# Kernel optimization log

Measured on AMD Instinct MI355X. Metric: run time of the kernel, lower is better.

Reference implementation:

```python
import jax, jax.numpy as jnp
import numpy as np

BN_EPS = 1e-5

def conv1x1(w, b, x):
    # w: [O, C], b: [O], x: [B, C, H, W] -> [B, O, H, W]
    return jnp.einsum('oc,bchw->bohw', w, x) + b[None, :, None, None]

def setup_inputs() -> dict:
    key = jax.random.key(0)
    ks = jax.random.split(key, 11)
    C, inter = 256, 128
    B, H, W = 16, 64, 32
    s = 0.05
    return {
        'x': jax.random.normal(ks[0], (B, C, H, W), jnp.float32),
        'g_w': jax.random.normal(ks[1], (inter, C), jnp.float32) * s,
        'g_b': jax.random.normal(ks[2], (inter,), jnp.float32) * s,
        'theta_w': jax.random.normal(ks[3], (inter, C), jnp.float32) * s,
        'theta_b': jax.random.normal(ks[4], (inter,), jnp.float32) * s,
        'phi_w': jax.random.normal(ks[5], (inter, C), jnp.float32) * s,
        'phi_b': jax.random.normal(ks[6], (inter,), jnp.float32) * s,
        'W_w': jax.random.normal(ks[7], (C, inter), jnp.float32) * s,
        'W_b': jax.random.normal(ks[8], (C,), jnp.float32) * s,
        'bn_gamma': jax.random.normal(ks[9], (C,), jnp.float32) * s,
        'bn_beta': jax.random.normal(ks[10], (C,), jnp.float32) * s,
    }

def reference(x, g_w, g_b, theta_w, theta_b, phi_w, phi_b, W_w, W_b, bn_gamma, bn_beta):
    B, C, H, W = x.shape
    N = H * W
    inter = g_w.shape[0]
    # 1x1 conv projections, flattened to token sequences
    g_x = conv1x1(g_w, g_b, x).reshape(B, inter, N).transpose(0, 2, 1)        # [B, N, inter]
    theta_x = conv1x1(theta_w, theta_b, x).reshape(B, inter, N).transpose(0, 2, 1)  # [B, N, inter]
    phi_x = conv1x1(phi_w, phi_b, x).reshape(B, inter, N)                      # [B, inter, N]
    # non-local attention: f = theta @ phi / N, then y = f @ g
    f_div_c = jnp.einsum('bnd,bdm->bnm', theta_x, phi_x) / N                   # [B, N, N]
    y = jnp.einsum('bnm,bmd->bnd', f_div_c, g_x)                               # [B, N, inter]
    y = y.transpose(0, 2, 1).reshape(B, inter, H, W)
    # W: 1x1 conv + BatchNorm (training-mode batch statistics)
    z = conv1x1(W_w, W_b, y)                                                   # [B, C, H, W]
    mean = jnp.mean(z, axis=(0, 2, 3), keepdims=True)
    var = jnp.var(z, axis=(0, 2, 3), keepdims=True)
    z_hat = (z - mean) * jax.lax.rsqrt(var + BN_EPS)
    z_bn = z_hat * bn_gamma[None, :, None, None] + bn_beta[None, :, None, None]
    return z_bn + x
```

## Files before the change

kernel.cpp:

```cpp
#include <hip/hip_runtime.h>

typedef unsigned int uint;
typedef unsigned short ushort;
typedef __attribute__((ext_vector_type(8))) short bf16x8;
typedef __attribute__((ext_vector_type(4))) float f32x4;

#define BB 16
#define CC 256
#define II 128
#define NN 2048
#define BN_EPS 1e-5f

#define OFF_GRAM   0
#define OFF_GPART  1048576
#define OFF_SPART  5242880
#define OFF_CP     5259264
#define OFF_STATP  5263360
#define OFF_STAT2  5394432
#define OFF_U      5394944
#define OFF_V      5396992
#define OFF_T1     5399040
#define OFF_KB     5923328
#define OFF_T2     6185472
#define OFF_FEND   6709760
#define USZ_SBF   (16*256*256)
#define USZ_X     (16*256*2048)

static __device__ __forceinline__ ushort f2bf(float f) {
    uint u = __float_as_uint(f);
    return (ushort)((u + 0x7FFFu + ((u >> 16) & 1u)) >> 16);
}
static __device__ __forceinline__ float bflo(uint w) { return __uint_as_float(w << 16); }
static __device__ __forceinline__ float bfhi(uint w) { return __uint_as_float(w & 0xFFFF0000u); }

#define MICRO_FMA(av, bv) \
    acc[0][0] += av.x * bv.x; acc[0][1] += av.x * bv.y; acc[0][2] += av.x * bv.z; acc[0][3] += av.x * bv.w; \
    acc[1][0] += av.y * bv.x; acc[1][1] += av.y * bv.y; acc[1][2] += av.y * bv.z; acc[1][3] += av.y * bv.w; \
    acc[2][0] += av.z * bv.x; acc[2][1] += av.z * bv.y; acc[2][2] += av.z * bv.z; acc[2][3] += av.z * bv.w; \
    acc[3][0] += av.w * bv.x; acc[3][1] += av.w * bv.y; acc[3][2] += av.w * bv.z; acc[3][3] += av.w * bv.w;

__global__ __launch_bounds__(256) void convert_transpose(
    const float* __restrict__ x, ushort* __restrict__ xbf, ushort* __restrict__ xT)
{
    __shared__ ushort tile[64][72];
    const int t = threadIdx.x;
    const int b = blockIdx.z, c0 = blockIdx.y * 64, n0 = blockIdx.x * 64;
    const int row = t & 63, ch = t >> 6;
    const size_t srcIdx = ((size_t)(b * CC + c0 + row)) * NN + n0 + ch * 16;
    const float4* sp = (const float4*)(x + srcIdx);
    float4 v0 = sp[0], v1 = sp[1], v2 = sp[2], v3 = sp[3];
    ushort a[16];
    a[0]=f2bf(v0.x); a[1]=f2bf(v0.y); a[2]=f2bf(v0.z); a[3]=f2bf(v0.w);
    a[4]=f2bf(v1.x); a[5]=f2bf(v1.y); a[6]=f2bf(v1.z); a[7]=f2bf(v1.w);
    a[8]=f2bf(v2.x); a[9]=f2bf(v2.y); a[10]=f2bf(v2.z); a[11]=f2bf(v2.w);
    a[12]=f2bf(v3.x); a[13]=f2bf(v3.y); a[14]=f2bf(v3.z); a[15]=f2bf(v3.w);
    uint p[8];
    #pragma unroll
    for (int i = 0; i < 8; ++i) p[i] = (uint)a[2*i] | ((uint)a[2*i+1] << 16);
    uint4* dp = (uint4*)(xbf + srcIdx);
    dp[0] = make_uint4(p[0], p[1], p[2], p[3]);
    dp[1] = make_uint4(p[4], p[5], p[6], p[7]);
    uint* tp = (uint*)&tile[row][ch * 16];
    #pragma unroll
    for (int i = 0; i < 8; ++i) tp[i] = p[i];
    __syncthreads();
    const int trow = t & 63, cch = t >> 6;
    uint q[8];
    #pragma unroll
    for (int i = 0; i < 8; ++i) {
        ushort lo = tile[cch * 16 + 2*i][trow];
        ushort hi = tile[cch * 16 + 2*i + 1][trow];
        q[i] = (uint)lo | ((uint)hi << 16);
    }
    uint4* op = (uint4*)(xT + ((size_t)(b * NN + n0 + trow)) * CC + c0 + cch * 16);
    op[0] = make_uint4(q[0], q[1], q[2], q[3]);
    op[1] = make_uint4(q[4], q[5], q[6], q[7]);
}

__global__ __launch_bounds__(256) void gram_mfma(
    const ushort* __restrict__ xbf, float* __restrict__ gpart, float* __restrict__ sPart)
{
    __shared__ ushort As[128][40];
    __shared__ ushort Bs[128][40];
    const int t = threadIdx.x;
    const int jt = blockIdx.x, it = blockIdx.y;
    const int b = blockIdx.z >> 2, kc = blockIdx.z & 3;
    const int iBase = it * 128, jBase = jt * 128;
    const int arow = t >> 1, ah = t & 1;
    const ushort* aSrc = xbf + ((size_t)(b * CC + iBase + arow)) * NN + kc * 512 + ah * 16;
    const ushort* bSrc = xbf + ((size_t)(b * CC + jBase + arow)) * NN + kc * 512 + ah * 16;
    const int lane = t & 63, wid = t >> 6;
    const int mb = (wid >> 1) * 64, nb = (wid & 1) * 64;
    const int lm = lane & 15, q = lane >> 4;
    f32x4 acc[4][4] = {};
    float ssum = 0.f;

    for (int it16 = 0; it16 < 16; ++it16) {
        const uint4* ap = (const uint4*)(aSrc + it16 * 32);
        uint4 a0 = ap[0], a1 = ap[1];
        const uint4* bp = (const uint4*)(bSrc + it16 * 32);
        uint4 b0 = bp[0], b1 = bp[1];
        *(uint4*)&As[arow][ah * 16] = a0;
        *(uint4*)&As[arow][ah * 16 + 8] = a1;
        *(uint4*)&Bs[arow][ah * 16] = b0;
        *(uint4*)&Bs[arow][ah * 16 + 8] = b1;
        if (jt == 0) {
            ssum += bflo(a0.x)+bfhi(a0.x)+bflo(a0.y)+bfhi(a0.y)
                  + bflo(a0.z)+bfhi(a0.z)+bflo(a0.w)+bfhi(a0.w)
                  + bflo(a1.x)+bfhi(a1.x)+bflo(a1.y)+bfhi(a1.y)
                  + bflo(a1.z)+bfhi(a1.z)+bflo(a1.w)+bfhi(a1.w);
        }
        __syncthreads();
        bf16x8 af[4], bf[4];
        #pragma unroll
        for (int mt = 0; mt < 4; ++mt)
            af[mt] = *(const bf16x8*)&As[mb + mt * 16 + lm][q * 8];
        #pragma unroll
        for (int nt = 0; nt < 4; ++nt)
            bf[nt] = *(const bf16x8*)&Bs[nb + nt * 16 + lm][q * 8];
        #pragma unroll
        for (int mt = 0; mt < 4; ++mt)
            #pragma unroll
            for (int nt = 0; nt < 4; ++nt)
                acc[mt][nt] = __builtin_amdgcn_mfma_f32_16x16x32_bf16(af[mt], bf[nt], acc[mt][nt], 0, 0, 0);
        __syncthreads();
    }
    float* gp = gpart + ((size_t)kc * BB + b) * CC * CC;
    #pragma unroll
    for (int mt = 0; mt < 4; ++mt)
        #pragma unroll
        for (int nt = 0; nt < 4; ++nt)
            #pragma unroll
            for (int r = 0; r < 4; ++r) {
                const int gi = iBase + mb + mt * 16 + q * 4 + r;
                const int gj = jBase + nb + nt * 16 + lm;
                gp[(size_t)gi * CC + gj] = acc[mt][nt][r];
            }
    if (jt == 0) {
        const float so = __shfl_xor(ssum, 1);
        if ((t & 1) == 0)
            sPart[((size_t)kc * BB + b) * CC + iBase + arow] = ssum + so;
    }
}

__global__ __launch_bounds__(256) void gram_reduce(
    const float* __restrict__ gpart, float* __restrict__ Gram)
{
    const int i = blockIdx.x * 256 + threadIdx.x;
    const size_t S = (size_t)BB * CC * CC / 4;
    const float4* p = reinterpret_cast<const float4*>(gpart);
    const float4 a = p[i], b = p[i + S], c = p[i + 2 * S], d = p[i + 3 * S];
    float4 o = { a.x + b.x + c.x + d.x, a.y + b.y + c.y + d.y,
                 a.z + b.z + c.z + d.z, a.w + b.w + c.w + d.w };
    reinterpret_cast<float4*>(Gram)[i] = o;
}

__global__ __launch_bounds__(256) void uv_kernel(
    const float* __restrict__ Gw, const float* __restrict__ Pw,
    const float* __restrict__ sPart, float* __restrict__ u, float* __restrict__ v)
{
    __shared__ float sLDS[256];
    const int b = blockIdx.x, t = threadIdx.x;
    sLDS[t] = sPart[(size_t)(0 * BB + b) * CC + t]
            + sPart[(size_t)(1 * BB + b) * CC + t]
            + sPart[(size_t)(2 * BB + b) * CC + t]
            + sPart[(size_t)(3 * BB + b) * CC + t];
    __syncthreads();
    const float* wrow = (t < 128) ? (Gw + (size_t)t * CC) : (Pw + (size_t)(t - 128) * CC);
    float acc = 0.f;
    for (int k = 0; k < CC; ++k) acc += wrow[k] * sLDS[k];
    if (t < 128) u[b * II + t] = acc;
    else         v[b * II + (t - 128)] = acc;
}

__global__ __launch_bounds__(256) void t1_gemm(
    const float* __restrict__ Gw, const float* __restrict__ Gram, float* __restrict__ T1)
{
    __shared__ float As[32][68];
    __shared__ float Bs[32][64];
    const int tid = threadIdx.x;
    const int jBase = blockIdx.x * 64, iBase = blockIdx.y * 64, b = blockIdx.z;
    const int a_r = tid >> 2, a_k = (tid & 3) * 8;
    const int b_n = tid & 63, b_k = tid >> 6;
    const int ty = tid >> 4, tx = tid & 15;
    float acc[4][4] = {};
    const float* ap0 = Gw + (size_t)(iBase + a_r) * CC + a_k;
    const float* bp0 = Gram + (size_t)b * CC * CC + jBase + b_n;
    for (int k0 = 0; k0 < CC; k0 += 32) {
        #pragma unroll
        for (int j = 0; j < 8; ++j) As[a_k + j][a_r] = ap0[k0 + j];
        #pragma unroll
        for (int kk = 0; kk < 8; ++kk) {
            const int k = b_k + kk * 4;
            Bs[k][b_n] = bp0[(size_t)(k0 + k) * CC];
        }
        __syncthreads();
        #pragma unroll
        for (int k = 0; k < 32; ++k) {
            const float4 av = *(const float4*)&As[k][ty * 4];
            const float4 bv = *(const float4*)&Bs[k][tx * 4];
            MICRO_FMA(av, bv)
        }
        __syncthreads();
    }
    float* dst = T1 + (size_t)b * II * CC;
    #pragma unroll
    for (int ii = 0; ii < 4; ++ii) {
        float4 o = { acc[ii][0], acc[ii][1], acc[ii][2], acc[ii][3] };
        *(float4*)&dst[(size_t)(iBase + ty * 4 + ii) * CC + jBase + tx * 4] = o;
    }
}

__global__ __launch_bounds__(256) void kb_gemm(
    const float* __restrict__ T1, const float* __restrict__ Pw,
    const float* __restrict__ u, const float* __restrict__ v,
    const float* __restrict__ gb, const float* __restrict__ pb,
    float* __restrict__ Kb)
{
    __shared__ float As[32][68];
    __shared__ float Bs[32][68];
    const int tid = threadIdx.x;
    const int jBase = blockIdx.x * 64, iBase = blockIdx.y * 64, b = blockIdx.z;
    const int a_r = tid >> 2, a_k = (tid & 3) * 8;
    const int ty = tid >> 4, tx = tid & 15;
    float acc[4][4] = {};
    const float* ap0 = T1 + (size_t)b * II * CC + (size_t)(iBase + a_r) * CC + a_k;
    const float* bp0 = Pw + (size_t)(jBase + a_r) * CC + a_k;
    for (int k0 = 0; k0 < CC; k0 += 32) {
        #pragma unroll
        for (int j = 0; j < 8; ++j) As[a_k + j][a_r] = ap0[k0 + j];
        #pragma unroll
        for (int j = 0; j < 8; ++j) Bs[a_k + j][a_r] = bp0[k0 + j];
        __syncthreads();
        #pragma unroll
        for (int k = 0; k < 32; ++k) {
            const float4 av = *(const float4*)&As[k][ty * 4];
            const float4 bv = *(const float4*)&Bs[k][tx * 4];
            MICRO_FMA(av, bv)
        }
        __syncthreads();
    }
    float* dst = Kb + (size_t)b * II * II;
    #pragma unroll
    for (int ii = 0; ii < 4; ++ii) {
        const int gi = iBase + ty * 4 + ii;
        const float ug = u[b * II + gi], gg = gb[gi];
        #pragma unroll
        for (int jj = 0; jj < 4; ++jj) {
            const int gj = jBase + tx * 4 + jj;
            acc[ii][jj] += ug * pb[gj] + gg * (v[b * II + gj] + (float)NN * pb[gj]);
        }
        float4 o = { acc[ii][0], acc[ii][1], acc[ii][2], acc[ii][3] };
        *(float4*)&dst[(size_t)gi * II + jBase + tx * 4] = o;
    }
}

__global__ __launch_bounds__(256) void t2_gemm(
    const float* __restrict__ Ww, const float* __restrict__ Kb, float* __restrict__ T2)
{
    __shared__ float As[32][68];
    __shared__ float Bs[32][64];
    const int tid = threadIdx.x;
    const int jBase = blockIdx.x * 64, iBase = blockIdx.y * 64, b = blockIdx.z;
    const int a_r = tid >> 2, a_k = (tid & 3) * 8;
    const int b_n = tid & 63, b_k = tid >> 6;
    const int ty = tid >> 4, tx = tid & 15;
    float acc[4][4] = {};
    const float* ap0 = Ww + (size_t)(iBase + a_r) * II + a_k;
    const float* bp0 = Kb + (size_t)b * II * II + jBase + b_n;
    for (int k0 = 0; k0 < II; k0 += 32) {
        #pragma unroll
        for (int j = 0; j < 8; ++j) As[a_k + j][a_r] = ap0[k0 + j];
        #pragma unroll
        for (int kk = 0; kk < 8; ++kk) {
            const int k = b_k + kk * 4;
            Bs[k][b_n] = bp0[(size_t)(k0 + k) * II];
        }
        __syncthreads();
        #pragma unroll
        for (int k = 0; k < 32; ++k) {
            const float4 av = *(const float4*)&As[k][ty * 4];
            const float4 bv = *(const float4*)&Bs[k][tx * 4];
            MICRO_FMA(av, bv)
        }
        __syncthreads();
    }
    float* dst = T2 + (size_t)b * CC * II;
    #pragma unroll
    for (int ii = 0; ii < 4; ++ii) {
        float4 o = { acc[ii][0], acc[ii][1], acc[ii][2], acc[ii][3] };
        *(float4*)&dst[(size_t)(iBase + ty * 4 + ii) * II + jBase + tx * 4] = o;
    }
}

__global__ __launch_bounds__(256) void s_gemm(
    const float* __restrict__ T2, const float* __restrict__ Tw,
    const float* __restrict__ tb, float* __restrict__ cprime,
    ushort* __restrict__ Sbf)
{
    __shared__ float As[32][68];
    __shared__ float Bs[32][64];
    const int tid = threadIdx.x;
    const int jBase = blockIdx.x * 64, iBase = blockIdx.y * 64, b = blockIdx.z;
    const int a_r = tid >> 2, a_k = (tid & 3) * 8;
    const int b_n = tid & 63, b_k = tid >> 6;
    const int ty = tid >> 4, tx = tid & 15;
    float acc[4][4] = {};
    float cp = 0.f;
    const float* ap0 = T2 + (size_t)b * CC * II + (size_t)(iBase + a_r) * II + a_k;
    const float* bp0 = Tw + jBase + b_n;
    for (int k0 = 0; k0 < II; k0 += 32) {
        #pragma unroll
        for (int j = 0; j < 8; ++j) {
            const float v = ap0[k0 + j];
            As[a_k + j][a_r] = v;
            if (blockIdx.x == 0) cp += v * tb[k0 + a_k + j];
        }
        #pragma unroll
        for (int kk = 0; kk < 8; ++kk) {
            const int k = b_k + kk * 4;
            Bs[k][b_n] = bp0[(size_t)(k0 + k) * CC];
        }
        __syncthreads();
        #pragma unroll
        for (int k = 0; k < 32; ++k) {
            const float4 av = *(const float4*)&As[k][ty * 4];
            const float4 bv = *(const float4*)&Bs[k][tx * 4];
            MICRO_FMA(av, bv)
        }
        __syncthreads();
    }
    const float sc = 1.0f / (float)NN;
    if (blockIdx.x == 0) {
        float c2 = cp + __shfl_xor(cp, 1);
        c2 += __shfl_xor(c2, 2);
        if ((tid & 3) == 0) cprime[b * CC + iBase + a_r] = c2 * sc;
    }
    ushort* dst = Sbf + (size_t)b * CC * CC;
    #pragma unroll
    for (int ii = 0; ii < 4; ++ii) {
        const int gi = iBase + ty * 4 + ii;
        uint p0 = (uint)f2bf(acc[ii][0] * sc) | ((uint)f2bf(acc[ii][1] * sc) << 16);
        uint p1 = (uint)f2bf(acc[ii][2] * sc) | ((uint)f2bf(acc[ii][3] * sc) << 16);
        uint2 o = { p0, p1 };
        *(uint2*)&dst[(size_t)gi * CC + jBase + tx * 4] = o;
    }
}

__global__ __launch_bounds__(256) void z_mfma(
    const ushort* __restrict__ Sbf, const ushort* __restrict__ xT,
    const float* __restrict__ cprime, ushort* __restrict__ zbf,
    float* __restrict__ statsPart)
{
    __shared__ ushort As[128][40];
    __shared__ ushort Bs[128][40];
    __shared__ float cpL[128];
    __shared__ float sSum[2][128], sSq[2][128];
    const int t = threadIdx.x;
    const int n0 = blockIdx.x * 128, ct = blockIdx.y * 128, b = blockIdx.z;
    const int arow = t >> 1, ah = t & 1;
    const ushort* aSrc = Sbf + ((size_t)(b * CC + ct + arow)) * CC + ah * 16;
    const ushort* bSrc = xT + ((size_t)(b * NN + n0 + arow)) * CC + ah * 16;
    const int lane = t & 63, wid = t >> 6;
    const int mb = (wid >> 1) * 64, nb = (wid & 1) * 64;
    const int lm = lane & 15, q = lane >> 4;
    f32x4 acc[4][4] = {};

    if (t < 128) cpL[t] = cprime[b * CC + ct + t];

    for (int k0 = 0; k0 < CC; k0 += 32) {
        const uint4* ap = (const uint4*)(aSrc + k0);
        uint4 a0 = ap[0], a1 = ap[1];
        const uint4* bp = (const uint4*)(bSrc + k0);
        uint4 b0 = bp[0], b1 = bp[1];
        *(uint4*)&As[arow][ah * 16] = a0;
        *(uint4*)&As[arow][ah * 16 + 8] = a1;
        *(uint4*)&Bs[arow][ah * 16] = b0;
        *(uint4*)&Bs[arow][ah * 16 + 8] = b1;
        __syncthreads();
        bf16x8 af[4], bf[4];
        #pragma unroll
        for (int mt = 0; mt < 4; ++mt)
            af[mt] = *(const bf16x8*)&As[mb + mt * 16 + lm][q * 8];
        #pragma unroll
        for (int nt = 0; nt < 4; ++nt)
            bf[nt] = *(const bf16x8*)&Bs[nb + nt * 16 + lm][q * 8];
        #pragma unroll
        for (int mt = 0; mt < 4; ++mt)
            #pragma unroll
            for (int nt = 0; nt < 4; ++nt)
                acc[mt][nt] = __builtin_amdgcn_mfma_f32_16x16x32_bf16(af[mt], bf[nt], acc[mt][nt], 0, 0, 0);
        __syncthreads();
    }
    const int nbw = wid & 1;
    #pragma unroll
    for (int mt = 0; mt < 4; ++mt) {
        #pragma unroll
        for (int r = 0; r < 4; ++r) {
            const int cl = mb + mt * 16 + q * 4 + r;
            const int ci = ct + cl;
            const float cp = cpL[cl];
            const size_t zrow = ((size_t)(b * CC + ci)) * NN;
            float s1 = 0.f, q1 = 0.f;
            #pragma unroll
            for (int nt = 0; nt < 4; ++nt) {
                const float val = acc[mt][nt][r] + cp;
                const int tok = n0 + nb + nt * 16 + lm;
                zbf[zrow + tok] = f2bf(val);
                s1 += val; q1 += val * val;
            }
            #pragma unroll
            for (int m = 1; m < 16; m <<= 1) {
                s1 += __shfl_xor(s1, m);
                q1 += __shfl_xor(q1, m);
            }
            if (lm == 0) { sSum[nbw][cl] = s1; sSq[nbw][cl] = q1; }
        }
    }
    __syncthreads();
    if (t < 128) {
        const int slot = blockIdx.z * 16 + blockIdx.x;
        statsPart[(size_t)slot * 512 + ct + t]       = sSum[0][t] + sSum[1][t];
        statsPart[(size_t)slot * 512 + 256 + ct + t] = sSq[0][t] + sSq[1][t];
    }
}

__global__ __launch_bounds__(512) void bn_finalize(
    const float* __restrict__ statsPart, float* __restrict__ stats2)
{
    __shared__ float red[512];
    const int t = threadIdx.x;
    float a = 0.f;
    for (int s = 0; s < 256; ++s) a += statsPart[(size_t)s * 512 + t];
    red[t] = a;
    __syncthreads();
    if (t < 256) {
        const float cnt = (float)(BB * NN);
        const float mean = red[t] / cnt;
        const float var = red[256 + t] / cnt - mean * mean;
        stats2[t] = mean;
        stats2[CC + t] = rsqrtf(var + BN_EPS);
    }
}

__global__ __launch_bounds__(256) void bn_apply(
    const ushort* __restrict__ zbf, const float* __restrict__ x,
    float* __restrict__ out, const float* __restrict__ stats2,
    const float* __restrict__ gamma, const float* __restrict__ beta)
{
    const size_t i = (size_t)blockIdx.x * 256 + threadIdx.x;
    const size_t base = i * 8;
    const int c = (int)((base >> 11) & (CC - 1));
    const float mean = stats2[c], istd = stats2[CC + c];
    const float gm = gamma[c] * istd;
    const float bt = beta[c] - mean * gm;
    const uint4 zz = *(const uint4*)(zbf + base);
    const float4 x0 = *(const float4*)(x + base);
    const float4 x1 = *(const float4*)(x + base + 4);
    float4 o0, o1;
    o0.x = bflo(zz.x) * gm + bt + x0.x;  o0.y = bfhi(zz.x) * gm + bt + x0.y;
    o0.z = bflo(zz.y) * gm + bt + x0.z;  o0.w = bfhi(zz.y) * gm + bt + x0.w;
    o1.x = bflo(zz.z) * gm + bt + x1.x;  o1.y = bfhi(zz.z) * gm + bt + x1.y;
    o1.z = bflo(zz.w) * gm + bt + x1.z;  o1.w = bfhi(zz.w) * gm + bt + x1.w;
    *(float4*)(out + base) = o0;
    *(float4*)(out + base + 4) = o1;
}

extern "C" void kernel_launch(void* const* d_in, const int* in_sizes, int n_in,
                              void* d_out, int out_size, void* d_ws, size_t ws_size,
                              hipStream_t stream) {
    const float* x    = (const float*)d_in[0];
    const float* g_w  = (const float*)d_in[1];
    const float* g_b  = (const float*)d_in[2];
    const float* th_w = (const float*)d_in[3];
    const float* th_b = (const float*)d_in[4];
    const float* ph_w = (const float*)d_in[5];
    const float* ph_b = (const float*)d_in[6];
    const float* W_w  = (const float*)d_in[7];
    const float* bn_g = (const float*)d_in[9];
    const float* bn_bt= (const float*)d_in[10];
    float* wsf = (float*)d_ws;
    float* out = (float*)d_out;

    ushort* SBF = (ushort*)(wsf + OFF_FEND);
    ushort* XBF = SBF + USZ_SBF;
    ushort* XT  = XBF + USZ_X;
    ushort* ZBF = XT + USZ_X;

    convert_transpose<<<dim3(32, 4, 16), 256, 0, stream>>>(x, XBF, XT);
    gram_mfma<<<dim3(2, 2, 64), 256, 0, stream>>>(XBF, wsf + OFF_GPART, wsf + OFF_SPART);
    gram_reduce<<<dim3(1024), 256, 0, stream>>>(wsf + OFF_GPART, wsf + OFF_GRAM);
    uv_kernel<<<dim3(16), 256, 0, stream>>>(g_w, ph_w, wsf + OFF_SPART, wsf + OFF_U, wsf + OFF_V);
    t1_gemm<<<dim3(4, 2, 16), 256, 0, stream>>>(g_w, wsf + OFF_GRAM, wsf + OFF_T1);
    kb_gemm<<<dim3(2, 2, 16), 256, 0, stream>>>(wsf + OFF_T1, ph_w, wsf + OFF_U, wsf + OFF_V,
                                                g_b, ph_b, wsf + OFF_KB);
    t2_gemm<<<dim3(2, 4, 16), 256, 0, stream>>>(W_w, wsf + OFF_KB, wsf + OFF_T2);
    s_gemm<<<dim3(4, 4, 16), 256, 0, stream>>>(wsf + OFF_T2, th_w, th_b, wsf + OFF_CP, SBF);
    z_mfma<<<dim3(16, 2, 16), 256, 0, stream>>>(SBF, XT, wsf + OFF_CP, ZBF, wsf + OFF_STATP);
    bn_finalize<<<dim3(1), 512, 0, stream>>>(wsf + OFF_STATP, wsf + OFF_STAT2);
    bn_apply<<<dim3(4096), 256, 0, stream>>>(ZBF, x, out, wsf + OFF_STAT2, bn_g, bn_bt);
}
```

Before: 229.9 us.

## Refactor low-rank chain into batch-independent weight products and bf16 MFMA GEMMs

Reorders the algebra of the collapsed attention chain. Weight-only products (W_w·g_w and theta^T·phi/N) and the bias terms are precomputed once in a small kernel, so the per-batch work becomes two bf16 MFMA GEMMs (H = F·Gram, then S = E·H) plus a fused vector kernel, replacing four fp32 SIMT GEMMs. The gram kernel now reads fp32 x directly and converts in registers, which drops the separate bf16 copy of x. The Gram matrix is stored in bf16, and bn_finalize reads with float4 across four row groups. The cost is more bf16 rounding in the intermediate products, which adds accuracy risk.

```diff
diff --git a/kernel.cpp b/kernel.cpp
--- a/kernel.cpp
+++ b/kernel.cpp
@@ -11,27 +11,36 @@
 #define NN 2048
 #define BN_EPS 1e-5f
 
-#define OFF_GRAM   0
-#define OFF_GPART  1048576
-#define OFF_SPART  5242880
-#define OFF_CP     5259264
-#define OFF_STATP  5263360
-#define OFF_STAT2  5394432
-#define OFF_U      5394944
-#define OFF_V      5396992
-#define OFF_T1     5399040
-#define OFF_KB     5923328
-#define OFF_T2     6185472
-#define OFF_FEND   6709760
-#define USZ_SBF   (16*256*256)
-#define USZ_X     (16*256*2048)
+#define OFF_GPART 0
+#define OFF_SPART 4194304
+#define OFF_CP    4210688
+#define OFF_STATP 4214784
+#define OFF_STAT2 4345856
+#define OFF_PT    4346368
+#define OFF_R1    4346624
+#define OFF_WGB   4346880
+#define OFF_ALPHA 4347136
+#define OFF_L1    4347152
+#define OFF_R2    4351248
+#define OFF_FEND  4355344
+#define UGRAM 0
+#define UE    1048576
+#define UFT   1114112
+#define UHT   1179648
+#define USBF  2228224
+#define UXT   3276800
+#define UZ    11665408
 
 static __device__ __forceinline__ ushort f2bf(float f) {
     uint u = __float_as_uint(f);
     return (ushort)((u + 0x7FFFu + ((u >> 16) & 1u)) >> 16);
 }
+static __device__ __forceinline__ uint pack2(float a, float b) {
+    return (uint)f2bf(a) | ((uint)f2bf(b) << 16);
+}
 static __device__ __forceinline__ float bflo(uint w) { return __uint_as_float(w << 16); }
 static __device__ __forceinline__ float bfhi(uint w) { return __uint_as_float(w & 0xFFFF0000u); }
+static __device__ __forceinline__ float bfu(ushort u) { return __uint_as_float((uint)u << 16); }
 
 #define MICRO_FMA(av, bv) \
     acc[0][0] += av.x * bv.x; acc[0][1] += av.x * bv.y; acc[0][2] += av.x * bv.z; acc[0][3] += av.x * bv.w; \
@@ -39,8 +48,8 @@
     acc[2][0] += av.z * bv.x; acc[2][1] += av.z * bv.y; acc[2][2] += av.z * bv.z; acc[2][3] += av.z * bv.w; \
     acc[3][0] += av.w * bv.x; acc[3][1] += av.w * bv.y; acc[3][2] += av.w * bv.z; acc[3][3] += av.w * bv.w;
 
-__global__ __launch_bounds__(256) void convert_transpose(
-    const float* __restrict__ x, ushort* __restrict__ xbf, ushort* __restrict__ xT)
+__global__ __launch_bounds__(256) void convert_xt(
+    const float* __restrict__ x, ushort* __restrict__ xT)
 {
     __shared__ ushort tile[64][72];
     const int t = threadIdx.x;
@@ -49,17 +58,11 @@
     const size_t srcIdx = ((size_t)(b * CC + c0 + row)) * NN + n0 + ch * 16;
     const float4* sp = (const float4*)(x + srcIdx);
     float4 v0 = sp[0], v1 = sp[1], v2 = sp[2], v3 = sp[3];
-    ushort a[16];
-    a[0]=f2bf(v0.x); a[1]=f2bf(v0.y); a[2]=f2bf(v0.z); a[3]=f2bf(v0.w);
-    a[4]=f2bf(v1.x); a[5]=f2bf(v1.y); a[6]=f2bf(v1.z); a[7]=f2bf(v1.w);
-    a[8]=f2bf(v2.x); a[9]=f2bf(v2.y); a[10]=f2bf(v2.z); a[11]=f2bf(v2.w);
-    a[12]=f2bf(v3.x); a[13]=f2bf(v3.y); a[14]=f2bf(v3.z); a[15]=f2bf(v3.w);
     uint p[8];
-    #pragma unroll
-    for (int i = 0; i < 8; ++i) p[i] = (uint)a[2*i] | ((uint)a[2*i+1] << 16);
-    uint4* dp = (uint4*)(xbf + srcIdx);
-    dp[0] = make_uint4(p[0], p[1], p[2], p[3]);
-    dp[1] = make_uint4(p[4], p[5], p[6], p[7]);
+    p[0] = pack2(v0.x, v0.y); p[1] = pack2(v0.z, v0.w);
+    p[2] = pack2(v1.x, v1.y); p[3] = pack2(v1.z, v1.w);
+    p[4] = pack2(v2.x, v2.y); p[5] = pack2(v2.z, v2.w);
+    p[6] = pack2(v3.x, v3.y); p[7] = pack2(v3.z, v3.w);
     uint* tp = (uint*)&tile[row][ch * 16];
     #pragma unroll
     for (int i = 0; i < 8; ++i) tp[i] = p[i];
@@ -78,7 +81,7 @@
 }
 
 __global__ __launch_bounds__(256) void gram_mfma(
-    const ushort* __restrict__ xbf, float* __restrict__ gpart, float* __restrict__ sPart)
+    const float* __restrict__ x, float* __restrict__ gpart, float* __restrict__ sPart)
 {
     __shared__ ushort As[128][40];
     __shared__ ushort Bs[128][40];
@@ -87,8 +90,8 @@
     const int b = blockIdx.z >> 2, kc = blockIdx.z & 3;
     const int iBase = it * 128, jBase = jt * 128;
     const int arow = t >> 1, ah = t & 1;
-    const ushort* aSrc = xbf + ((size_t)(b * CC + iBase + arow)) * NN + kc * 512 + ah * 16;
-    const ushort* bSrc = xbf + ((size_t)(b * CC + jBase + arow)) * NN + kc * 512 + ah * 16;
+    const float* aSrc = x + ((size_t)(b * CC + iBase + arow)) * NN + kc * 512 + ah * 16;
+    const float* bSrc = x + ((size_t)(b * CC + jBase + arow)) * NN + kc * 512 + ah * 16;
     const int lane = t & 63, wid = t >> 6;
     const int mb = (wid >> 1) * 64, nb = (wid & 1) * 64;
     const int lm = lane & 15, q = lane >> 4;
@@ -96,19 +99,21 @@
     float ssum = 0.f;
 
     for (int it16 = 0; it16 < 16; ++it16) {
-        const uint4* ap = (const uint4*)(aSrc + it16 * 32);
-        uint4 a0 = ap[0], a1 = ap[1];
-        const uint4* bp = (const uint4*)(bSrc + it16 * 32);
-        uint4 b0 = bp[0], b1 = bp[1];
-        *(uint4*)&As[arow][ah * 16] = a0;
-        *(uint4*)&As[arow][ah * 16 + 8] = a1;
-        *(uint4*)&Bs[arow][ah * 16] = b0;
-        *(uint4*)&Bs[arow][ah * 16 + 8] = b1;
+        const float4* ap = (const float4*)(aSrc + it16 * 32);
+        float4 a0 = ap[0], a1 = ap[1], a2 = ap[2], a3 = ap[3];
+        const float4* bp = (const float4*)(bSrc + it16 * 32);
+        float4 b0 = bp[0], b1 = bp[1], b2 = bp[2], b3 = bp[3];
+        uint4 pa0 = { pack2(a0.x,a0.y), pack2(a0.z,a0.w), pack2(a1.x,a1.y), pack2(a1.z,a1.w) };
+        uint4 pa1 = { pack2(a2.x,a2.y), pack2(a2.z,a2.w), pack2(a3.x,a3.y), pack2(a3.z,a3.w) };
+        uint4 pb0 = { pack2(b0.x,b0.y), pack2(b0.z,b0.w), pack2(b1.x,b1.y), pack2(b1.z,b1.w) };
+        uint4 pb1 = { pack2(b2.x,b2.y), pack2(b2.z,b2.w), pack2(b3.x,b3.y), pack2(b3.z,b3.w) };
+        *(uint4*)&As[arow][ah * 16]     = pa0;
+        *(uint4*)&As[arow][ah * 16 + 8] = pa1;
+        *(uint4*)&Bs[arow][ah * 16]     = pb0;
+        *(uint4*)&Bs[arow][ah * 16 + 8] = pb1;
         if (jt == 0) {
-            ssum += bflo(a0.x)+bfhi(a0.x)+bflo(a0.y)+bfhi(a0.y)
-                  + bflo(a0.z)+bfhi(a0.z)+bflo(a0.w)+bfhi(a0.w)
-                  + bflo(a1.x)+bfhi(a1.x)+bflo(a1.y)+bfhi(a1.y)
-                  + bflo(a1.z)+bfhi(a1.z)+bflo(a1.w)+bfhi(a1.w);
+            ssum += a0.x+a0.y+a0.z+a0.w + a1.x+a1.y+a1.z+a1.w
+                  + a2.x+a2.y+a2.z+a2.w + a3.x+a3.y+a3.z+a3.w;
         }
         __syncthreads();
         bf16x8 af[4], bf[4];
@@ -144,207 +149,273 @@
 }
 
 __global__ __launch_bounds__(256) void gram_reduce(
-    const float* __restrict__ gpart, float* __restrict__ Gram)
+    const float* __restrict__ gpart, ushort* __restrict__ GramBF)
 {
     const int i = blockIdx.x * 256 + threadIdx.x;
     const size_t S = (size_t)BB * CC * CC / 4;
-    const float4* p = reinterpret_cast<const float4*>(gpart);
+    const float4* p = (const float4*)gpart;
     const float4 a = p[i], b = p[i + S], c = p[i + 2 * S], d = p[i + 3 * S];
     float4 o = { a.x + b.x + c.x + d.x, a.y + b.y + c.y + d.y,
                  a.z + b.z + c.z + d.z, a.w + b.w + c.w + d.w };
-    reinterpret_cast<float4*>(Gram)[i] = o;
-}
-
-__global__ __launch_bounds__(256) void uv_kernel(
-    const float* __restrict__ Gw, const float* __restrict__ Pw,
-    const float* __restrict__ sPart, float* __restrict__ u, float* __restrict__ v)
-{
-    __shared__ float sLDS[256];
-    const int b = blockIdx.x, t = threadIdx.x;
-    sLDS[t] = sPart[(size_t)(0 * BB + b) * CC + t]
-            + sPart[(size_t)(1 * BB + b) * CC + t]
-            + sPart[(size_t)(2 * BB + b) * CC + t]
-            + sPart[(size_t)(3 * BB + b) * CC + t];
-    __syncthreads();
-    const float* wrow = (t < 128) ? (Gw + (size_t)t * CC) : (Pw + (size_t)(t - 128) * CC);
-    float acc = 0.f;
-    for (int k = 0; k < CC; ++k) acc += wrow[k] * sLDS[k];
-    if (t < 128) u[b * II + t] = acc;
-    else         v[b * II + (t - 128)] = acc;
-}
-
-__global__ __launch_bounds__(256) void t1_gemm(
-    const float* __restrict__ Gw, const float* __restrict__ Gram, float* __restrict__ T1)
-{
+    uint2 pk = { pack2(o.x, o.y), pack2(o.z, o.w) };
+    ((uint2*)GramBF)[i] = pk;
+}
+
+__global__ __launch_bounds__(256) void w1_kernel(
+    const float* __restrict__ Ww, const float* __restrict__ Gw,
+    const float* __restrict__ Pw, const float* __restrict__ Tw,
+    const float* __restrict__ gb, const float* __restrict__ pb, const float* __restrict__ tb,
+    ushort* __restrict__ EBF, ushort* __restrict__ FT,
+    float* __restrict__ pt, float* __restrict__ r1, float* __restrict__ wgb,
+    float* __restrict__ alpha)
+{
+    const int bz = blockIdx.x;
+    const int tid = threadIdx.x;
+    if (bz == 32) {
+        const int t = tid;
+        float ptv = 0.f, r1v = 0.f, wgbv = 0.f;
+        for (int d = 0; d < II; ++d) {
+            ptv  += Pw[(size_t)d * CC + t] * tb[d];
+            r1v  += Tw[(size_t)d * CC + t] * pb[d];
+            wgbv += Ww[(size_t)t * II + d] * gb[d];
+        }
+        pt[t] = ptv; r1[t] = r1v; wgb[t] = wgbv;
+        if (t == 0) {
+            float al = 0.f;
+            for (int d = 0; d < II; ++d) al += pb[d] * tb[d];
+            alpha[0] = al;
+        }
+        return;
+    }
     __shared__ float As[32][68];
-    __shared__ float Bs[32][64];
-    const int tid = threadIdx.x;
-    const int jBase = blockIdx.x * 64, iBase = blockIdx.y * 64, b = blockIdx.z;
+    __shared__ float Bs[32][68];
     const int a_r = tid >> 2, a_k = (tid & 3) * 8;
     const int b_n = tid & 63, b_k = tid >> 6;
     const int ty = tid >> 4, tx = tid & 15;
     float acc[4][4] = {};
-    const float* ap0 = Gw + (size_t)(iBase + a_r) * CC + a_k;
-    const float* bp0 = Gram + (size_t)b * CC * CC + jBase + b_n;
+    if (bz < 16) {
+        const int cBase = (bz >> 2) * 64, iBase = (bz & 3) * 64;
+        const float* ap0 = Ww + (size_t)(cBase + a_r) * II + a_k;
+        const float* bp0 = Gw + iBase + b_n;
+        for (int k0 = 0; k0 < II; k0 += 32) {
+            #pragma unroll
+            for (int j = 0; j < 8; ++j) As[a_k + j][a_r] = ap0[k0 + j];
+            #pragma unroll
+            for (int kk = 0; kk < 8; ++kk) {
+                const int k = b_k + kk * 4;
+                Bs[k][b_n] = bp0[(size_t)(k0 + k) * CC];
+            }
+            __syncthreads();
+            #pragma unroll
+            for (int k = 0; k < 32; ++k) {
+                const float4 av = *(const float4*)&As[k][ty * 4];
+                const float4 bv = *(const float4*)&Bs[k][tx * 4];
+                MICRO_FMA(av, bv)
+            }
+            __syncthreads();
+        }
+        #pragma unroll
+        for (int ii = 0; ii < 4; ++ii) {
+            uint2 o = { pack2(acc[ii][0], acc[ii][1]), pack2(acc[ii][2], acc[ii][3]) };
+            *(uint2*)&EBF[(size_t)(cBase + ty * 4 + ii) * CC + iBase + tx * 4] = o;
+        }
+    } else {
+        const int z = bz - 16;
+        const int jBase = (z >> 2) * 64, kBase = (z & 3) * 64;
+        const float* ap0 = Tw + jBase + b_n;
+        const float* bp0 = Pw + kBase + b_n;
+        for (int k0 = 0; k0 < II; k0 += 32) {
+            #pragma unroll
+            for (int kk = 0; kk < 8; ++kk) {
+                const int k = b_k + kk * 4;
+                As[k][b_n] = ap0[(size_t)(k0 + k) * CC];
+                Bs[k][b_n] = bp0[(size_t)(k0 + k) * CC];
+            }
+            __syncthreads();
+            #pragma unroll
+            for (int k = 0; k < 32; ++k) {
+                const float4 av = *(const float4*)&As[k][ty * 4];
+                const float4 bv = *(const float4*)&Bs[k][tx * 4];
+                MICRO_FMA(av, bv)
+            }
+            __syncthreads();
+        }
+        const float sc = 1.0f / (float)NN;
+        #pragma unroll
+        for (int ii = 0; ii < 4; ++ii) {
+            uint2 o = { pack2(acc[ii][0]*sc, acc[ii][1]*sc), pack2(acc[ii][2]*sc, acc[ii][3]*sc) };
+            *(uint2*)&FT[(size_t)(jBase + ty * 4 + ii) * CC + kBase + tx * 4] = o;
+        }
+    }
+}
+
+__global__ __launch_bounds__(256) void u_kernel(
+    const float* __restrict__ sPart, const ushort* __restrict__ GramBF,
+    const ushort* __restrict__ EBF, const ushort* __restrict__ FT,
+    const float* __restrict__ pt, const float* __restrict__ r1,
+    const float* __restrict__ wgb, const float* __restrict__ alpha,
+    float* __restrict__ cprime, float* __restrict__ L1, float* __restrict__ R2)
+{
+    __shared__ float sL[256], ptL[256], GptL[256], red[256];
+    const int b = blockIdx.x, t = threadIdx.x;
+    sL[t] = sPart[(size_t)(0 * BB + b) * CC + t] + sPart[(size_t)(1 * BB + b) * CC + t]
+          + sPart[(size_t)(2 * BB + b) * CC + t] + sPart[(size_t)(3 * BB + b) * CC + t];
+    ptL[t] = pt[t];
+    __syncthreads();
+    red[t] = sL[t] * ptL[t];
+    __syncthreads();
+    for (int s = 128; s > 0; s >>= 1) {
+        if (t < s) red[t] += red[t + s];
+        __syncthreads();
+    }
+    const float spt = red[0];
+    {
+        const uint4* gp = (const uint4*)(GramBF + ((size_t)b * CC + t) * CC);
+        float g = 0.f;
+        #pragma unroll 4
+        for (int kk = 0; kk < 32; ++kk) {
+            uint4 v = gp[kk]; const int k = kk * 8;
+            g += bflo(v.x)*ptL[k]   + bfhi(v.x)*ptL[k+1] + bflo(v.y)*ptL[k+2] + bfhi(v.y)*ptL[k+3]
+               + bflo(v.z)*ptL[k+4] + bfhi(v.z)*ptL[k+5] + bflo(v.w)*ptL[k+6] + bfhi(v.w)*ptL[k+7];
+        }
+        GptL[t] = g;
+    }
+    __syncthreads();
+    float es = 0.f, eg = 0.f;
+    {
+        const uint4* ep = (const uint4*)(EBF + (size_t)t * CC);
+        #pragma unroll 4
+        for (int kk = 0; kk < 32; ++kk) {
+            uint4 v = ep[kk]; const int k = kk * 8;
+            float e0=bflo(v.x),e1=bfhi(v.x),e2=bflo(v.y),e3=bfhi(v.y);
+            float e4=bflo(v.z),e5=bfhi(v.z),e6=bflo(v.w),e7=bfhi(v.w);
+            es += e0*sL[k]+e1*sL[k+1]+e2*sL[k+2]+e3*sL[k+3]+e4*sL[k+4]+e5*sL[k+5]+e6*sL[k+6]+e7*sL[k+7];
+            eg += e0*GptL[k]+e1*GptL[k+1]+e2*GptL[k+2]+e3*GptL[k+3]+e4*GptL[k+4]+e5*GptL[k+5]+e6*GptL[k+6]+e7*GptL[k+7];
+        }
+    }
+    float r2 = 0.f;
+    {
+        const uint4* fp = (const uint4*)(FT + (size_t)t * CC);
+        #pragma unroll 4
+        for (int kk = 0; kk < 32; ++kk) {
+            uint4 v = fp[kk]; const int k = kk * 8;
+            r2 += bflo(v.x)*sL[k]   + bfhi(v.x)*sL[k+1] + bflo(v.y)*sL[k+2] + bfhi(v.y)*sL[k+3]
+                + bflo(v.z)*sL[k+4] + bfhi(v.z)*sL[k+5] + bflo(v.w)*sL[k+6] + bfhi(v.w)*sL[k+7];
+        }
+    }
+    const float al = alpha[0];
+    const float wg = wgb[t];
+    cprime[b * CC + t] = (eg + al * es + spt * wg) / (float)NN + al * wg;
+    L1[b * CC + t] = es / (float)NN;
+    R2[b * CC + t] = r2 + r1[t];
+}
+
+__global__ __launch_bounds__(256) void h_mfma(
+    const ushort* __restrict__ FT, const ushort* __restrict__ GramBF,
+    ushort* __restrict__ HT)
+{
+    __shared__ ushort As[128][40];
+    __shared__ ushort Bs[128][40];
+    const int t = threadIdx.x;
+    const int iBase = blockIdx.x * 128, jBase = blockIdx.y * 128, b = blockIdx.z;
+    const int arow = t >> 1, ah = t & 1;
+    const ushort* aSrc = FT + (size_t)(jBase + arow) * CC + ah * 16;
+    const ushort* bSrc = GramBF + ((size_t)b * CC + iBase + arow) * CC + ah * 16;
+    const int lane = t & 63, wid = t >> 6;
+    const int mb = (wid >> 1) * 64, nb = (wid & 1) * 64;
+    const int lm = lane & 15, q = lane >> 4;
+    f32x4 acc[4][4] = {};
     for (int k0 = 0; k0 < CC; k0 += 32) {
-        #pragma unroll
-        for (int j = 0; j < 8; ++j) As[a_k + j][a_r] = ap0[k0 + j];
-        #pragma unroll
-        for (int kk = 0; kk < 8; ++kk) {
-            const int k = b_k + kk * 4;
-            Bs[k][b_n] = bp0[(size_t)(k0 + k) * CC];
-        }
-        __syncthreads();
-        #pragma unroll
-        for (int k = 0; k < 32; ++k) {
-            const float4 av = *(const float4*)&As[k][ty * 4];
-            const float4 bv = *(const float4*)&Bs[k][tx * 4];
-            MICRO_FMA(av, bv)
-        }
-        __syncthreads();
-    }
-    float* dst = T1 + (size_t)b * II * CC;
-    #pragma unroll
-    for (int ii = 0; ii < 4; ++ii) {
-        float4 o = { acc[ii][0], acc[ii][1], acc[ii][2], acc[ii][3] };
-        *(float4*)&dst[(size_t)(iBase + ty * 4 + ii) * CC + jBase + tx * 4] = o;
-    }
-}
-
-__global__ __launch_bounds__(256) void kb_gemm(
-    const float* __restrict__ T1, const float* __restrict__ Pw,
-    const float* __restrict__ u, const float* __restrict__ v,
-    const float* __restrict__ gb, const float* __restrict__ pb,
-    float* __restrict__ Kb)
-{
-    __shared__ float As[32][68];
-    __shared__ float Bs[32][68];
-    const int tid = threadIdx.x;
-    const int jBase = blockIdx.x * 64, iBase = blockIdx.y * 64, b = blockIdx.z;
-    const int a_r = tid >> 2, a_k = (tid & 3) * 8;
-    const int ty = tid >> 4, tx = tid & 15;
-    float acc[4][4] = {};
-    const float* ap0 = T1 + (size_t)b * II * CC + (size_t)(iBase + a_r) * CC + a_k;
-    const float* bp0 = Pw + (size_t)(jBase + a_r) * CC + a_k;
+        *(uint4*)&As[arow][ah * 16]     = ((const uint4*)(aSrc + k0))[0];
+        *(uint4*)&As[arow][ah * 16 + 8] = ((const uint4*)(aSrc + k0))[1];
+        *(uint4*)&Bs[arow][ah * 16]     = ((const uint4*)(bSrc + k0))[0];
+        *(uint4*)&Bs[arow][ah * 16 + 8] = ((const uint4*)(bSrc + k0))[1];
+        __syncthreads();
+        bf16x8 af[4], bf[4];
+        #pragma unroll
+        for (int mt = 0; mt < 4; ++mt)
+            af[mt] = *(const bf16x8*)&As[mb + mt * 16 + lm][q * 8];
+        #pragma unroll
+        for (int nt = 0; nt < 4; ++nt)
+            bf[nt] = *(const bf16x8*)&Bs[nb + nt * 16 + lm][q * 8];
+        #pragma unroll
+        for (int mt = 0; mt < 4; ++mt)
+            #pragma unroll
+            for (int nt = 0; nt < 4; ++nt)
+                acc[mt][nt] = __builtin_amdgcn_mfma_f32_16x16x32_bf16(af[mt], bf[nt], acc[mt][nt], 0, 0, 0);
+        __syncthreads();
+    }
+    ushort* dst = HT + (size_t)b * CC * CC;
+    #pragma unroll
+    for (int mt = 0; mt < 4; ++mt)
+        #pragma unroll
+        for (int r = 0; r < 4; ++r) {
+            const int j = jBase + mb + mt * 16 + q * 4 + r;
+            #pragma unroll
+            for (int nt = 0; nt < 4; ++nt) {
+                const int i = iBase + nb + nt * 16 + lm;
+                dst[(size_t)j * CC + i] = f2bf(acc[mt][nt][r]);
+            }
+        }
+}
+
+__global__ __launch_bounds__(256) void s2_mfma(
+    const ushort* __restrict__ EBF, const ushort* __restrict__ HT,
+    const float* __restrict__ r1, const float* __restrict__ R2,
+    const float* __restrict__ L1, const float* __restrict__ wgb,
+    ushort* __restrict__ Sbf)
+{
+    __shared__ ushort As[128][40];
+    __shared__ ushort Bs[128][40];
+    const int t = threadIdx.x;
+    const int jBase = blockIdx.x * 128, cBase = blockIdx.y * 128, b = blockIdx.z;
+    const int arow = t >> 1, ah = t & 1;
+    const ushort* aSrc = EBF + (size_t)(cBase + arow) * CC + ah * 16;
+    const ushort* bSrc = HT + ((size_t)b * CC + jBase + arow) * CC + ah * 16;
+    const int lane = t & 63, wid = t >> 6;
+    const int mb = (wid >> 1) * 64, nb = (wid & 1) * 64;
+    const int lm = lane & 15, q = lane >> 4;
+    f32x4 acc[4][4] = {};
     for (int k0 = 0; k0 < CC; k0 += 32) {
-        #pragma unroll
-        for (int j = 0; j < 8; ++j) As[a_k + j][a_r] = ap0[k0 + j];
-        #pragma unroll
-        for (int j = 0; j < 8; ++j) Bs[a_k + j][a_r] = bp0[k0 + j];
-        __syncthreads();
-        #pragma unroll
-        for (int k = 0; k < 32; ++k) {
-            const float4 av = *(const float4*)&As[k][ty * 4];
-            const float4 bv = *(const float4*)&Bs[k][tx * 4];
-            MICRO_FMA(av, bv)
-        }
-        __syncthreads();
-    }
-    float* dst = Kb + (size_t)b * II * II;
-    #pragma unroll
-    for (int ii = 0; ii < 4; ++ii) {
-        const int gi = iBase + ty * 4 + ii;
-        const float ug = u[b * II + gi], gg = gb[gi];
-        #pragma unroll
-        for (int jj = 0; jj < 4; ++jj) {
-            const int gj = jBase + tx * 4 + jj;
-            acc[ii][jj] += ug * pb[gj] + gg * (v[b * II + gj] + (float)NN * pb[gj]);
-        }
-        float4 o = { acc[ii][0], acc[ii][1], acc[ii][2], acc[ii][3] };
-        *(float4*)&dst[(size_t)gi * II + jBase + tx * 4] = o;
-    }
-}
-
-__global__ __launch_bounds__(256) void t2_gemm(
-    const float* __restrict__ Ww, const float* __restrict__ Kb, float* __restrict__ T2)
-{
-    __shared__ float As[32][68];
-    __shared__ float Bs[32][64];
-    const int tid = threadIdx.x;
-    const int jBase = blockIdx.x * 64, iBase = blockIdx.y * 64, b = blockIdx.z;
-    const int a_r = tid >> 2, a_k = (tid & 3) * 8;
-    const int b_n = tid & 63, b_k = tid >> 6;
-    const int ty = tid >> 4, tx = tid & 15;
-    float acc[4][4] = {};
-    const float* ap0 = Ww + (size_t)(iBase + a_r) * II + a_k;
-    const float* bp0 = Kb + (size_t)b * II * II + jBase + b_n;
-    for (int k0 = 0; k0 < II; k0 += 32) {
-        #pragma unroll
-        for (int j = 0; j < 8; ++j) As[a_k + j][a_r] = ap0[k0 + j];
-        #pragma unroll
-        for (int kk = 0; kk < 8; ++kk) {
-            const int k = b_k + kk * 4;
-            Bs[k][b_n] = bp0[(size_t)(k0 + k) * II];
-        }
-        __syncthreads();
-        #pragma unroll
-        for (int k = 0; k < 32; ++k) {
-            const float4 av = *(const float4*)&As[k][ty * 4];
-            const float4 bv = *(const float4*)&Bs[k][tx * 4];
-            MICRO_FMA(av, bv)
-        }
-        __syncthreads();
-    }
-    float* dst = T2 + (size_t)b * CC * II;
-    #pragma unroll
-    for (int ii = 0; ii < 4; ++ii) {
-        float4 o = { acc[ii][0], acc[ii][1], acc[ii][2], acc[ii][3] };
-        *(float4*)&dst[(size_t)(iBase + ty * 4 + ii) * II + jBase + tx * 4] = o;
-    }
-}
-
-__global__ __launch_bounds__(256) void s_gemm(
-    const float* __restrict__ T2, const float* __restrict__ Tw,
-    const float* __restrict__ tb, float* __restrict__ cprime,
-    ushort* __restrict__ Sbf)
-{
-    __shared__ float As[32][68];
-    __shared__ float Bs[32][64];
-    const int tid = threadIdx.x;
-    const int jBase = blockIdx.x * 64, iBase = blockIdx.y * 64, b = blockIdx.z;
-    const int a_r = tid >> 2, a_k = (tid & 3) * 8;
-    const int b_n = tid & 63, b_k = tid >> 6;
-    const int ty = tid >> 4, tx = tid & 15;
-    float acc[4][4] = {};
-    float cp = 0.f;
-    const float* ap0 = T2 + (size_t)b * CC * II + (size_t)(iBase + a_r) * II + a_k;
-    const float* bp0 = Tw + jBase + b_n;
-    for (int k0 = 0; k0 < II; k0 += 32) {
-        #pragma unroll
-        for (int j = 0; j < 8; ++j) {
-            const float v = ap0[k0 + j];
-            As[a_k + j][a_r] = v;
-            if (blockIdx.x == 0) cp += v * tb[k0 + a_k + j];
-        }
-        #pragma unroll
-        for (int kk = 0; kk < 8; ++kk) {
-            const int k = b_k + kk * 4;
-            Bs[k][b_n] = bp0[(size_t)(k0 + k) * CC];
-        }
-        __syncthreads();
-        #pragma unroll
-        for (int k = 0; k < 32; ++k) {
-            const float4 av = *(const float4*)&As[k][ty * 4];
-            const float4 bv = *(const float4*)&Bs[k][tx * 4];
-            MICRO_FMA(av, bv)
-        }
-        __syncthreads();
-    }
-    const float sc = 1.0f / (float)NN;
-    if (blockIdx.x == 0) {
-        float c2 = cp + __shfl_xor(cp, 1);
-        c2 += __shfl_xor(c2, 2);
-        if ((tid & 3) == 0) cprime[b * CC + iBase + a_r] = c2 * sc;
+        *(uint4*)&As[arow][ah * 16]     = ((const uint4*)(aSrc + k0))[0];
+        *(uint4*)&As[arow][ah * 16 + 8] = ((const uint4*)(aSrc + k0))[1];
+        *(uint4*)&Bs[arow][ah * 16]     = ((const uint4*)(bSrc + k0))[0];
+        *(uint4*)&Bs[arow][ah * 16 + 8] = ((const uint4*)(bSrc + k0))[1];
+        __syncthreads();
+        bf16x8 af[4], bf[4];
+        #pragma unroll
+        for (int mt = 0; mt < 4; ++mt)
+            af[mt] = *(const bf16x8*)&As[mb + mt * 16 + lm][q * 8];
+        #pragma unroll
+        for (int nt = 0; nt < 4; ++nt)
+            bf[nt] = *(const bf16x8*)&Bs[nb + nt * 16 + lm][q * 8];
+        #pragma unroll
+        for (int mt = 0; mt < 4; ++mt)
+            #pragma unroll
+            for (int nt = 0; nt < 4; ++nt)
+                acc[mt][nt] = __builtin_amdgcn_mfma_f32_16x16x32_bf16(af[mt], bf[nt], acc[mt][nt], 0, 0, 0);
+        __syncthreads();
+    }
+    float r1v[4], R2v[4];
+    #pragma unroll
+    for (int nt = 0; nt < 4; ++nt) {
+        const int j = jBase + nb + nt * 16 + lm;
+        r1v[nt] = r1[j];
+        R2v[nt] = R2[b * CC + j];
     }
     ushort* dst = Sbf + (size_t)b * CC * CC;
     #pragma unroll
-    for (int ii = 0; ii < 4; ++ii) {
-        const int gi = iBase + ty * 4 + ii;
-        uint p0 = (uint)f2bf(acc[ii][0] * sc) | ((uint)f2bf(acc[ii][1] * sc) << 16);
-        uint p1 = (uint)f2bf(acc[ii][2] * sc) | ((uint)f2bf(acc[ii][3] * sc) << 16);
-        uint2 o = { p0, p1 };
-        *(uint2*)&dst[(size_t)gi * CC + jBase + tx * 4] = o;
-    }
+    for (int mt = 0; mt < 4; ++mt)
+        #pragma unroll
+        for (int r = 0; r < 4; ++r) {
+            const int c = cBase + mb + mt * 16 + q * 4 + r;
+            const float l1v = L1[b * CC + c], wgv = wgb[c];
+            #pragma unroll
+            for (int nt = 0; nt < 4; ++nt) {
+                const int j = jBase + nb + nt * 16 + lm;
+                dst[(size_t)c * CC + j] = f2bf(acc[mt][nt][r] + l1v * r1v[nt] + wgv * R2v[nt]);
+            }
+        }
 }
 
 __global__ __launch_bounds__(256) void z_mfma(
@@ -369,14 +440,10 @@
     if (t < 128) cpL[t] = cprime[b * CC + ct + t];
 
     for (int k0 = 0; k0 < CC; k0 += 32) {
-        const uint4* ap = (const uint4*)(aSrc + k0);
-        uint4 a0 = ap[0], a1 = ap[1];
-        const uint4* bp = (const uint4*)(bSrc + k0);
-        uint4 b0 = bp[0], b1 = bp[1];
-        *(uint4*)&As[arow][ah * 16] = a0;
-        *(uint4*)&As[arow][ah * 16 + 8] = a1;
-        *(uint4*)&Bs[arow][ah * 16] = b0;
-        *(uint4*)&Bs[arow][ah * 16 + 8] = b1;
+        *(uint4*)&As[arow][ah * 16]     = ((const uint4*)(aSrc + k0))[0];
+        *(uint4*)&As[arow][ah * 16 + 8] = ((const uint4*)(aSrc + k0))[1];
+        *(uint4*)&Bs[arow][ah * 16]     = ((const uint4*)(bSrc + k0))[0];
+        *(uint4*)&Bs[arow][ah * 16 + 8] = ((const uint4*)(bSrc + k0))[1];
         __syncthreads();
         bf16x8 af[4], bf[4];
         #pragma unroll
@@ -428,16 +495,29 @@
 __global__ __launch_bounds__(512) void bn_finalize(
     const float* __restrict__ statsPart, float* __restrict__ stats2)
 {
-    __shared__ float red[512];
-    const int t = threadIdx.x;
-    float a = 0.f;
-    for (int s = 0; s < 256; ++s) a += statsPart[(size_t)s * 512 + t];
-    red[t] = a;
+    __shared__ float4 red4[4][128];
+    __shared__ float sf[512];
+    const int t = threadIdx.x, col = t & 127, grp = t >> 7;
+    const float4* sp4 = (const float4*)statsPart;
+    float4 a = { 0.f, 0.f, 0.f, 0.f };
+    for (int s = grp; s < 256; s += 4) {
+        float4 v = sp4[(size_t)s * 128 + col];
+        a.x += v.x; a.y += v.y; a.z += v.z; a.w += v.w;
+    }
+    red4[grp][col] = a;
+    __syncthreads();
+    if (t < 128) {
+        float4 t0 = red4[0][t], t1 = red4[1][t], t2 = red4[2][t], t3 = red4[3][t];
+        sf[t*4+0] = t0.x + t1.x + t2.x + t3.x;
+        sf[t*4+1] = t0.y + t1.y + t2.y + t3.y;
+        sf[t*4+2] = t0.z + t1.z + t2.z + t3.z;
+        sf[t*4+3] = t0.w + t1.w + t2.w + t3.w;
+    }
     __syncthreads();
     if (t < 256) {
         const float cnt = (float)(BB * NN);
-        const float mean = red[t] / cnt;
-        const float var = red[256 + t] / cnt - mean * mean;
+        const float mean = sf[t] / cnt;
+        const float var = sf[256 + t] / cnt - mean * mean;
         stats2[t] = mean;
         stats2[CC + t] = rsqrtf(var + BN_EPS);
     }
@@ -481,22 +561,21 @@
     const float* bn_bt= (const float*)d_in[10];
     float* wsf = (float*)d_ws;
     float* out = (float*)d_out;
-
-    ushort* SBF = (ushort*)(wsf + OFF_FEND);
-    ushort* XBF = SBF + USZ_SBF;
-    ushort* XT  = XBF + USZ_X;
-    ushort* ZBF = XT + USZ_X;
-
-    convert_transpose<<<dim3(32, 4, 16), 256, 0, stream>>>(x, XBF, XT);
-    gram_mfma<<<dim3(2, 2, 64), 256, 0, stream>>>(XBF, wsf + OFF_GPART, wsf + OFF_SPART);
-    gram_reduce<<<dim3(1024), 256, 0, stream>>>(wsf + OFF_GPART, wsf + OFF_GRAM);
-    uv_kernel<<<dim3(16), 256, 0, stream>>>(g_w, ph_w, wsf + OFF_SPART, wsf + OFF_U, wsf + OFF_V);
-    t1_gemm<<<dim3(4, 2, 16), 256, 0, stream>>>(g_w, wsf + OFF_GRAM, wsf + OFF_T1);
-    kb_gemm<<<dim3(2, 2, 16), 256, 0, stream>>>(wsf + OFF_T1, ph_w, wsf + OFF_U, wsf + OFF_V,
-                                                g_b, ph_b, wsf + OFF_KB);
-    t2_gemm<<<dim3(2, 4, 16), 256, 0, stream>>>(W_w, wsf + OFF_KB, wsf + OFF_T2);
-    s_gemm<<<dim3(4, 4, 16), 256, 0, stream>>>(wsf + OFF_T2, th_w, th_b, wsf + OFF_CP, SBF);
-    z_mfma<<<dim3(16, 2, 16), 256, 0, stream>>>(SBF, XT, wsf + OFF_CP, ZBF, wsf + OFF_STATP);
+    ushort* ub = (ushort*)(wsf + OFF_FEND);
+
+    gram_mfma<<<dim3(2, 2, 64), 256, 0, stream>>>(x, wsf + OFF_GPART, wsf + OFF_SPART);
+    convert_xt<<<dim3(32, 4, 16), 256, 0, stream>>>(x, ub + UXT);
+    gram_reduce<<<dim3(1024), 256, 0, stream>>>(wsf + OFF_GPART, ub + UGRAM);
+    w1_kernel<<<dim3(33), 256, 0, stream>>>(W_w, g_w, ph_w, th_w, g_b, ph_b, th_b,
+        ub + UE, ub + UFT, wsf + OFF_PT, wsf + OFF_R1, wsf + OFF_WGB, wsf + OFF_ALPHA);
+    u_kernel<<<dim3(16), 256, 0, stream>>>(wsf + OFF_SPART, ub + UGRAM, ub + UE, ub + UFT,
+        wsf + OFF_PT, wsf + OFF_R1, wsf + OFF_WGB, wsf + OFF_ALPHA,
+        wsf + OFF_CP, wsf + OFF_L1, wsf + OFF_R2);
+    h_mfma<<<dim3(2, 2, 16), 256, 0, stream>>>(ub + UFT, ub + UGRAM, ub + UHT);
+    s2_mfma<<<dim3(2, 2, 16), 256, 0, stream>>>(ub + UE, ub + UHT,
+        wsf + OFF_R1, wsf + OFF_R2, wsf + OFF_L1, wsf + OFF_WGB, ub + USBF);
+    z_mfma<<<dim3(16, 2, 16), 256, 0, stream>>>(ub + USBF, ub + UXT,
+        wsf + OFF_CP, ub + UZ, wsf + OFF_STATP);
     bn_finalize<<<dim3(1), 512, 0, stream>>>(wsf + OFF_STATP, wsf + OFF_STAT2);
-    bn_apply<<<dim3(4096), 256, 0, stream>>>(ZBF, x, out, wsf + OFF_STAT2, bn_g, bn_bt);
-}
+    bn_apply<<<dim3(4096), 256, 0, stream>>>(ub + UZ, x, out, wsf + OFF_STAT2, bn_g, bn_bt);
+}
```

After: 225.3 us. -2.0%, faster.
